# Kernel optimization log

Measured on AMD Instinct MI355X. Metric: run time of the kernel, lower is better.

## Reference

```python
import jax, jax.numpy as jnp
import numpy as np

B, N, H, W = 128, 8192, 7, 7


def setup_inputs() -> dict:
    key = jax.random.key(0)
    ks = jax.random.split(key, 10)
    inp = {
        'x': jax.random.normal(ks[0], (B, N, H, W), dtype=jnp.float32),
        'y': jax.random.normal(ks[1], (B, N), dtype=jnp.float32),
        # nn.MultiheadAttention(embed_dim=1, num_heads=1) params (all scalar)
        'wq': jax.random.normal(ks[2], (), dtype=jnp.float32),
        'wk': jax.random.normal(ks[3], (), dtype=jnp.float32),
        'wv': jax.random.normal(ks[4], (), dtype=jnp.float32),
        'bq': jax.random.normal(ks[5], (), dtype=jnp.float32) * 0.1,
        'bk': jax.random.normal(ks[6], (), dtype=jnp.float32) * 0.1,
        'bv': jax.random.normal(ks[7], (), dtype=jnp.float32) * 0.1,
        'wo': jax.random.normal(ks[8], (), dtype=jnp.float32),
        'bo': jax.random.normal(ks[9], (), dtype=jnp.float32) * 0.1,
    }
    return inp


def _mha1(q_src, kv_src, wq, bq, wk, bk, wv, bv, wo, bo):
    # embed_dim=1, num_heads=1, scale = 1/sqrt(1) = 1.
    # torch sees (seq=B, batch=N, embed=1): attention mixes the B axis per n.
    q = q_src * wq + bq            # [B, N]
    k = kv_src * wk + bk           # [B, N]
    v = kv_src * wv + bv           # [B, N]
    scores = jnp.einsum('in,jn->ijn', q, k)      # [B, B, N]
    a = jax.nn.softmax(scores, axis=1)           # softmax over keys j
    out = jnp.einsum('ijn,jn->in', a, v)         # [B, N]
    return out * wo + bo


def reference(x, y, wq, bq, wk, bk, wv, bv, wo, bo):
    xp = jnp.mean(x, axis=(2, 3))                # AdaptiveAvgPool2d((1,1)) -> [B, N]
    self_x = _mha1(xp, xp, wq, bq, wk, bk, wv, bv, wo, bo)
    self_y = _mha1(y, y, wq, bq, wk, bk, wv, bv, wo, bo)
    cross_x = _mha1(xp, y, wq, bq, wk, bk, wv, bv, wo, bo)
    cross_y = _mha1(y, xp, wq, bq, wk, bk, wv, bv, wo, bo)
    f_x = xp + self_x
    f_y = y + self_y
    c_f_x = cross_x + f_x
    c_f_y = cross_y + f_y
    return jnp.concatenate((c_f_x, c_f_y), axis=1)   # [B, 2N]
```

## Files before the change

kernel.cpp:

```cpp
#include <hip/hip_runtime.h>


constexpr int B_SEQ = 128;
constexpr int N_COL = 8192;
constexpr int HWP   = 49;
constexpr int NT    = 256;
constexpr int TC    = 4;
constexpr int VSTR  = 132;
constexpr int OSTR  = 5;

typedef float v2f __attribute__((ext_vector_type(2)));

#if __has_builtin(__builtin_elementwise_fma)
#define VFMA(a, b, c) __builtin_elementwise_fma((a), (b), (c))
#else
__device__ __forceinline__ v2f VFMA(v2f a, v2f b, v2f c) {
    v2f r; r.x = fmaf(a.x, b.x, c.x); r.y = fmaf(a.y, b.y, c.y); return r;
}
#endif

__global__ __launch_bounds__(NT, 5) void rsca_fused(
    const float* __restrict__ x, const float* __restrict__ y,
    const float* __restrict__ pwq, const float* __restrict__ pwk,
    const float* __restrict__ pwv, const float* __restrict__ pbq,
    const float* __restrict__ pbk, const float* __restrict__ pbv,
    const float* __restrict__ pwo, const float* __restrict__ pbo,
    float* __restrict__ out)
{
    __shared__ float xv[TC * VSTR];
    __shared__ float yv[TC * VSTR];
    __shared__ float pmnx[8][TC], pmxx[8][TC];
    __shared__ float pmny[4][TC], pmxy[4][TC];
    __shared__ float obuf[2][B_SEQ * OSTR];

    const int t    = threadIdx.x;
    const int bid  = blockIdx.x;
    const int cg = (bid & 7) * ((N_COL / TC) >> 3) + (bid >> 3);
    const int n0 = cg * TC;

    const int ql   = t & 3;
    const int seg  = t >> 2;
    const int lane = t & 63;
    const int wid  = t >> 6;

    const float wq = pwq[0], wk = pwk[0], wv = pwv[0];
    const float bq = pbq[0], bk = pbk[0], bv = pbv[0];
    const float wo = pwo[0], bo = pbo[0];
    const float L2E = 1.4426950408889634f;
    const float wkL = wk * L2E, bkL = bk * L2E;
    const float alpha = wo * wv;
    const float beta2 = 2.0f * (wo * bv + bo);

    {
        const int j = t >> 2, c = t & 3;
        const float fy0 = y[(size_t)j * N_COL + n0 + c];
        const float fy1 = y[(size_t)(j + 64) * N_COL + n0 + c];
        yv[c * VSTR + j]      = fy0;
        yv[c * VSTR + j + 64] = fy1;
        float mn = fminf(fy0, fy1), mx = fmaxf(fy0, fy1);
        #pragma unroll
        for (int off = 4; off <= 32; off <<= 1) {
            mn = fminf(mn, __shfl_xor(mn, off));
            mx = fmaxf(mx, __shfl_xor(mx, off));
        }
        if (lane < 4) { pmny[wid][lane] = mn; pmxy[wid][lane] = mx; }
    }

    for (int pass = 0; pass < 2; ++pass) {
        const int j = pass * 64 + seg;
        const float4* __restrict__ base =
            (const float4*)(x + ((size_t)j * N_COL + n0) * (size_t)HWP);
        float4 v[13];
        #pragma unroll
        for (int k = 0; k < 12; ++k) v[k] = base[ql + 4 * k];
        v[12] = base[48];

        float s0 = 0.f, s1 = 0.f, s2 = 0.f, s3 = 0.f;
        s0 += v[0].x + v[0].y + v[0].z + v[0].w;
        s0 += v[1].x + v[1].y + v[1].z + v[1].w;
        s0 += v[2].x + v[2].y + v[2].z + v[2].w;
        s1 += v[4].x + v[4].y + v[4].z + v[4].w;
        s1 += v[5].x + v[5].y + v[5].z + v[5].w;
        s2 += v[7].x + v[7].y + v[7].z + v[7].w;
        s2 += v[8].x + v[8].y + v[8].z + v[8].w;
        s3 += v[10].x + v[10].y + v[10].z + v[10].w;
        s3 += v[11].x + v[11].y + v[11].z + v[11].w;
        { const float sm = v[3].x + v[3].y + v[3].z + v[3].w;
          const float cr = (ql == 0) ? v[3].x : 0.0f;
          s0 += cr; s1 += sm - cr; }
        { const float sm = v[6].x + v[6].y + v[6].z + v[6].w;
          const float cr = (ql == 0) ? (v[6].x + v[6].y) : 0.0f;
          s1 += cr; s2 += sm - cr; }
        { const float sm = v[9].x + v[9].y + v[9].z + v[9].w;
          const float cr = (ql == 0) ? (v[9].x + v[9].y + v[9].z) : 0.0f;
          s2 += cr; s3 += sm - cr; }
        const float tail = v[12].x + v[12].y + v[12].z + v[12].w;

        s0 += __shfl_xor(s0, 1); s1 += __shfl_xor(s1, 1);
        s2 += __shfl_xor(s2, 1); s3 += __shfl_xor(s3, 1);
        s0 += __shfl_xor(s0, 2); s1 += __shfl_xor(s1, 2);
        s2 += __shfl_xor(s2, 2); s3 += __shfl_xor(s3, 2);
        float r = s0;
        r = (ql == 1) ? s1 : r;
        r = (ql == 2) ? s2 : r;
        r = (ql == 3) ? (s3 + tail) : r;
        const float mean = r * (1.0f / HWP);
        xv[ql * VSTR + j] = mean;

        float mn = mean, mx = mean;
        #pragma unroll
        for (int off = 4; off <= 32; off <<= 1) {
            mn = fminf(mn, __shfl_xor(mn, off));
            mx = fmaxf(mx, __shfl_xor(mx, off));
        }
        if (lane < 4) {
            pmnx[pass * 4 + wid][lane] = mn;
            pmxx[pass * 4 + wid][lane] = mx;
        }
    }
    __syncthreads();

    const int i  = t & (B_SEQ - 1);
    const int ch = t >> 7;
    #pragma unroll
    for (int cc = 0; cc < 2; ++cc) {
        const int c = ch * 2 + cc;
        const float* __restrict__ vx = &xv[c * VSTR];
        const float* __restrict__ vy = &yv[c * VSTR];

        float vxmn = pmnx[0][c], vxmx = pmxx[0][c];
        #pragma unroll
        for (int s = 1; s < 8; ++s) {
            vxmn = fminf(vxmn, pmnx[s][c]);
            vxmx = fmaxf(vxmx, pmxx[s][c]);
        }
        float vymn = pmny[0][c], vymx = pmxy[0][c];
        #pragma unroll
        for (int s = 1; s < 4; ++s) {
            vymn = fminf(vymn, pmny[s][c]);
            vymx = fmaxf(vymx, pmxy[s][c]);
        }
        const float axv = fmaf(vxmx, wkL, bkL), bxv = fmaf(vxmn, wkL, bkL);
        const float kxmx = fmaxf(axv, bxv), kxmn = fminf(axv, bxv);
        const float ayv = fmaf(vymx, wkL, bkL), byv = fmaf(vymn, wkL, bkL);
        const float kymx = fmaxf(ayv, byv), kymn = fminf(ayv, byv);

        const float xi = vx[i], yi = vy[i];
        const float qx = fmaf(xi, wq, bq), qy = fmaf(yi, wq, bq);
        const float nmsx = -(qx >= 0.f ? qx * kxmx : qx * kxmn);
        const float nmcy = -(qy >= 0.f ? qy * kxmx : qy * kxmn);
        const float nmsy = -(qy >= 0.f ? qy * kymx : qy * kymn);
        const float nmcx = -(qx >= 0.f ? qx * kymx : qx * kymn);

        const float qxw = qx * wkL, qyw = qy * wkL;
        const v2f qxw2 = {qxw, qxw}, qyw2 = {qyw, qyw};
        const float csx = fmaf(qx, bkL, nmsx), ccy = fmaf(qy, bkL, nmcy);
        const float csy = fmaf(qy, bkL, nmsy), ccx = fmaf(qx, bkL, nmcx);
        const v2f csx2 = {csx, csx}, ccy2 = {ccy, ccy};
        const v2f csy2 = {csy, csy}, ccx2 = {ccx, ccx};

        v2f s0sx = {0.f, 0.f}, s1sx = {0.f, 0.f};
        v2f s0cy = {0.f, 0.f}, s1cy = {0.f, 0.f};
        v2f s0sy = {0.f, 0.f}, s1sy = {0.f, 0.f};
        v2f s0cx = {0.f, 0.f}, s1cx = {0.f, 0.f};

        auto px2 = [&](float v0, float v1) {
            const v2f vvj = {v0, v1};
            v2f t1 = VFMA(qxw2, vvj, csx2);
            v2f e1; e1.x = __builtin_amdgcn_exp2f(t1.x);
                    e1.y = __builtin_amdgcn_exp2f(t1.y);
            s1sx = VFMA(e1, vvj, s1sx); s0sx += e1;
            v2f t2 = VFMA(qyw2, vvj, ccy2);
            v2f e2; e2.x = __builtin_amdgcn_exp2f(t2.x);
                    e2.y = __builtin_amdgcn_exp2f(t2.y);
            s1cy = VFMA(e2, vvj, s1cy); s0cy += e2;
        };
        auto py2 = [&](float v0, float v1) {
            const v2f vvj = {v0, v1};
            v2f t3 = VFMA(qyw2, vvj, csy2);
            v2f e3; e3.x = __builtin_amdgcn_exp2f(t3.x);
                    e3.y = __builtin_amdgcn_exp2f(t3.y);
            s1sy = VFMA(e3, vvj, s1sy); s0sy += e3;
            v2f t4 = VFMA(qxw2, vvj, ccx2);
            v2f e4; e4.x = __builtin_amdgcn_exp2f(t4.x);
                    e4.y = __builtin_amdgcn_exp2f(t4.y);
            s1cx = VFMA(e4, vvj, s1cx); s0cx += e4;
        };

        float4 a0 = *(const float4*)&vx[0], a1 = *(const float4*)&vx[4];
        float4 b0 = *(const float4*)&vy[0], b1 = *(const float4*)&vy[4];
        for (int j0 = 0; j0 < B_SEQ; j0 += 8) {
            const int jn = (j0 + 8) & (B_SEQ - 1);
            float4 na0 = *(const float4*)&vx[jn];
            float4 na1 = *(const float4*)&vx[jn + 4];
            float4 nb0 = *(const float4*)&vy[jn];
            float4 nb1 = *(const float4*)&vy[jn + 4];

            px2(a0.x, a0.y); px2(a0.z, a0.w); px2(a1.x, a1.y); px2(a1.z, a1.w);
            py2(b0.x, b0.y); py2(b0.z, b0.w); py2(b1.x, b1.y); py2(b1.z, b1.w);

            a0 = na0; a1 = na1; b0 = nb0; b1 = nb1;
        }
        const float S0sx = s0sx.x + s0sx.y, S1sx = s1sx.x + s1sx.y;
        const float S0cy = s0cy.x + s0cy.y, S1cy = s1cy.x + s1cy.y;
        const float S0sy = s0sy.x + s0sy.y, S1sy = s1sy.x + s1sy.y;
        const float S0cx = s0cx.x + s0cx.y, S1cx = s1cx.x + s1cx.y;
        const float mx_attn = S1sx * __builtin_amdgcn_rcpf(S0sx)
                            + S1cx * __builtin_amdgcn_rcpf(S0cx);
        const float my_attn = S1sy * __builtin_amdgcn_rcpf(S0sy)
                            + S1cy * __builtin_amdgcn_rcpf(S0cy);
        obuf[0][i * OSTR + c] = fmaf(alpha, mx_attn, beta2 + xi);
        obuf[1][i * OSTR + c] = fmaf(alpha, my_attn, beta2 + yi);
    }
    __syncthreads();

    {
        const int set = t >> 7;
        const int ii  = t & (B_SEQ - 1);
        const float* p = &obuf[set][ii * OSTR];
        float4 val;
        val.x = p[0]; val.y = p[1]; val.z = p[2]; val.w = p[3];
        *(float4*)&out[(size_t)ii * (2 * N_COL) + (size_t)set * N_COL + n0] = val;
    }
}

extern "C" void kernel_launch(void* const* d_in, const int* in_sizes, int n_in,
                              void* d_out, int out_size, void* d_ws, size_t ws_size,
                              hipStream_t stream) {
    const float* x   = (const float*)d_in[0];
    const float* y   = (const float*)d_in[1];
    const float* pwq = (const float*)d_in[2];
    const float* pwk = (const float*)d_in[3];
    const float* pwv = (const float*)d_in[4];
    const float* pbq = (const float*)d_in[5];
    const float* pbk = (const float*)d_in[6];
    const float* pbv = (const float*)d_in[7];
    const float* pwo = (const float*)d_in[8];
    const float* pbo = (const float*)d_in[9];
    float* out = (float*)d_out;

    rsca_fused<<<dim3(N_COL / TC), dim3(NT), 0, stream>>>(
        x, y, pwq, pwk, pwv, pbq, pbk, pbv, pwo, pbo, out);
}
```

Measured before the change: 322.9 us.

## Warp-specialize kernel into producer load waves and consumer attention waves

Each 512-thread block now handles two 4-column groups. Four producer wavefronts load and pool x and y into double-buffered shared memory and signal readiness through workgroup-scope atomic counters. Four consumer wavefronts spin-wait on those counters, compute the attention sums, and write the outputs. The aim is to overlap global-memory loads with the exp-heavy softmax compute inside one block. In exchange it uses spin-wait synchronization, fewer blocks, and lower per-block occupancy, and because each buffer is used only once the overlap is limited to the two groups.

```diff
diff --git a/kernel.cpp b/kernel.cpp
--- a/kernel.cpp
+++ b/kernel.cpp
@@ -4,8 +4,10 @@
 constexpr int B_SEQ = 128;
 constexpr int N_COL = 8192;
 constexpr int HWP   = 49;
-constexpr int NT    = 256;
+constexpr int NT    = 512;
 constexpr int TC    = 4;
+constexpr int NG    = 2;
+constexpr int CPB   = TC * NG;
 constexpr int VSTR  = 132;
 constexpr int OSTR  = 5;
 
@@ -19,7 +21,7 @@
 }
 #endif
 
-__global__ __launch_bounds__(NT, 5) void rsca_fused(
+__global__ __launch_bounds__(NT, 4) void rsca_ws(
     const float* __restrict__ x, const float* __restrict__ y,
     const float* __restrict__ pwq, const float* __restrict__ pwk,
     const float* __restrict__ pwv, const float* __restrict__ pbq,
@@ -27,21 +29,21 @@
     const float* __restrict__ pwo, const float* __restrict__ pbo,
     float* __restrict__ out)
 {
-    __shared__ float xv[TC * VSTR];
-    __shared__ float yv[TC * VSTR];
-    __shared__ float pmnx[8][TC], pmxx[8][TC];
-    __shared__ float pmny[4][TC], pmxy[4][TC];
-    __shared__ float obuf[2][B_SEQ * OSTR];
+    __shared__ float kvx[2][TC * VSTR];
+    __shared__ float kvy[2][TC * VSTR];
+    __shared__ float pmnx[2][8][TC], pmxx[2][8][TC];
+    __shared__ float pmny[2][4][TC], pmxy[2][4][TC];
+    __shared__ float obuf[2][2][B_SEQ * OSTR];
+    __shared__ int   rdy[2], dne[2];
 
     const int t    = threadIdx.x;
     const int bid  = blockIdx.x;
-    const int cg = (bid & 7) * ((N_COL / TC) >> 3) + (bid >> 3);
-    const int n0 = cg * TC;
-
-    const int ql   = t & 3;
-    const int seg  = t >> 2;
     const int lane = t & 63;
-    const int wid  = t >> 6;
+    const int cg = (bid & 7) * ((N_COL / CPB) >> 3) + (bid >> 3);
+    const int n0 = cg * CPB;
+
+    if (t == 0) { rdy[0] = rdy[1] = 0; dne[0] = dne[1] = 0; }
+    __syncthreads();
 
     const float wq = pwq[0], wk = pwk[0], wv = pwv[0];
     const float bq = pbq[0], bk = pbk[0], bv = pbv[0];
@@ -51,176 +53,203 @@
     const float alpha = wo * wv;
     const float beta2 = 2.0f * (wo * bv + bo);
 
-    {
-        const int j = t >> 2, c = t & 3;
-        const float fy0 = y[(size_t)j * N_COL + n0 + c];
-        const float fy1 = y[(size_t)(j + 64) * N_COL + n0 + c];
-        yv[c * VSTR + j]      = fy0;
-        yv[c * VSTR + j + 64] = fy1;
-        float mn = fminf(fy0, fy1), mx = fmaxf(fy0, fy1);
+    if (t < 256) {
+        const int ql  = t & 3;
+        const int seg = t >> 2;
+        const int wid = t >> 6;
+        for (int g = 0; g < NG; ++g) {
+            const int s  = g & 1;
+            const int c0 = n0 + g * TC;
+            {
+                const float fy0 = y[(size_t)seg * N_COL + c0 + ql];
+                const float fy1 = y[(size_t)(seg + 64) * N_COL + c0 + ql];
+                kvy[s][ql * VSTR + seg]      = fy0;
+                kvy[s][ql * VSTR + seg + 64] = fy1;
+                float mn = fminf(fy0, fy1), mx = fmaxf(fy0, fy1);
+                #pragma unroll
+                for (int off = 4; off <= 32; off <<= 1) {
+                    mn = fminf(mn, __shfl_xor(mn, off));
+                    mx = fmaxf(mx, __shfl_xor(mx, off));
+                }
+                if (lane < 4) { pmny[s][wid][lane] = mn; pmxy[s][wid][lane] = mx; }
+            }
+            for (int pass = 0; pass < 2; ++pass) {
+                const int j = pass * 64 + seg;
+                const float4* __restrict__ base =
+                    (const float4*)(x + ((size_t)j * N_COL + c0) * (size_t)HWP);
+                float4 v[13];
+                #pragma unroll
+                for (int k = 0; k < 12; ++k) v[k] = base[ql + 4 * k];
+                v[12] = base[48];
+
+                float s0 = 0.f, s1 = 0.f, s2 = 0.f, s3 = 0.f;
+                s0 += v[0].x + v[0].y + v[0].z + v[0].w;
+                s0 += v[1].x + v[1].y + v[1].z + v[1].w;
+                s0 += v[2].x + v[2].y + v[2].z + v[2].w;
+                s1 += v[4].x + v[4].y + v[4].z + v[4].w;
+                s1 += v[5].x + v[5].y + v[5].z + v[5].w;
+                s2 += v[7].x + v[7].y + v[7].z + v[7].w;
+                s2 += v[8].x + v[8].y + v[8].z + v[8].w;
+                s3 += v[10].x + v[10].y + v[10].z + v[10].w;
+                s3 += v[11].x + v[11].y + v[11].z + v[11].w;
+                { const float sm = v[3].x + v[3].y + v[3].z + v[3].w;
+                  const float cr = (ql == 0) ? v[3].x : 0.0f;
+                  s0 += cr; s1 += sm - cr; }
+                { const float sm = v[6].x + v[6].y + v[6].z + v[6].w;
+                  const float cr = (ql == 0) ? (v[6].x + v[6].y) : 0.0f;
+                  s1 += cr; s2 += sm - cr; }
+                { const float sm = v[9].x + v[9].y + v[9].z + v[9].w;
+                  const float cr = (ql == 0) ? (v[9].x + v[9].y + v[9].z) : 0.0f;
+                  s2 += cr; s3 += sm - cr; }
+                const float tail = v[12].x + v[12].y + v[12].z + v[12].w;
+
+                s0 += __shfl_xor(s0, 1); s1 += __shfl_xor(s1, 1);
+                s2 += __shfl_xor(s2, 1); s3 += __shfl_xor(s3, 1);
+                s0 += __shfl_xor(s0, 2); s1 += __shfl_xor(s1, 2);
+                s2 += __shfl_xor(s2, 2); s3 += __shfl_xor(s3, 2);
+                float r = s0;
+                r = (ql == 1) ? s1 : r;
+                r = (ql == 2) ? s2 : r;
+                r = (ql == 3) ? (s3 + tail) : r;
+                const float mean = r * (1.0f / HWP);
+                kvx[s][ql * VSTR + j] = mean;
+
+                float mn = mean, mx = mean;
+                #pragma unroll
+                for (int off = 4; off <= 32; off <<= 1) {
+                    mn = fminf(mn, __shfl_xor(mn, off));
+                    mx = fmaxf(mx, __shfl_xor(mx, off));
+                }
+                if (lane < 4) {
+                    pmnx[s][pass * 4 + wid][lane] = mn;
+                    pmxx[s][pass * 4 + wid][lane] = mx;
+                }
+            }
+            if (lane == 0)
+                __hip_atomic_fetch_add(&rdy[s], 1, __ATOMIC_RELEASE,
+                                       __HIP_MEMORY_SCOPE_WORKGROUP);
+        }
+    } else {
+        const int tc = t - 256;
+        const int i  = tc & (B_SEQ - 1);
+        const int ch = tc >> 7;
+        for (int g = 0; g < NG; ++g) {
+            const int s   = g & 1;
+            const int tgt = 4 * (g / 2 + 1);
+            while (__hip_atomic_load(&rdy[s], __ATOMIC_ACQUIRE,
+                                     __HIP_MEMORY_SCOPE_WORKGROUP) < tgt)
+                __builtin_amdgcn_s_sleep(2);
+
+            #pragma unroll
+            for (int cc = 0; cc < 2; ++cc) {
+                const int c = ch * 2 + cc;
+                const float* __restrict__ vx = &kvx[s][c * VSTR];
+                const float* __restrict__ vy = &kvy[s][c * VSTR];
+
+                float vxmn = pmnx[s][0][c], vxmx = pmxx[s][0][c];
+                #pragma unroll
+                for (int p = 1; p < 8; ++p) {
+                    vxmn = fminf(vxmn, pmnx[s][p][c]);
+                    vxmx = fmaxf(vxmx, pmxx[s][p][c]);
+                }
+                float vymn = pmny[s][0][c], vymx = pmxy[s][0][c];
+                #pragma unroll
+                for (int p = 1; p < 4; ++p) {
+                    vymn = fminf(vymn, pmny[s][p][c]);
+                    vymx = fmaxf(vymx, pmxy[s][p][c]);
+                }
+                const float axv = fmaf(vxmx, wkL, bkL), bxv = fmaf(vxmn, wkL, bkL);
+                const float kxmx = fmaxf(axv, bxv), kxmn = fminf(axv, bxv);
+                const float ayv = fmaf(vymx, wkL, bkL), byv = fmaf(vymn, wkL, bkL);
+                const float kymx = fmaxf(ayv, byv), kymn = fminf(ayv, byv);
+
+                const float xi = vx[i], yi = vy[i];
+                const float qx = fmaf(xi, wq, bq), qy = fmaf(yi, wq, bq);
+                const float nmsx = -(qx >= 0.f ? qx * kxmx : qx * kxmn);
+                const float nmcy = -(qy >= 0.f ? qy * kxmx : qy * kxmn);
+                const float nmsy = -(qy >= 0.f ? qy * kymx : qy * kymn);
+                const float nmcx = -(qx >= 0.f ? qx * kymx : qx * kymn);
+
+                const float qxw = qx * wkL, qyw = qy * wkL;
+                const v2f qxw2 = {qxw, qxw}, qyw2 = {qyw, qyw};
+                const float csx = fmaf(qx, bkL, nmsx), ccy = fmaf(qy, bkL, nmcy);
+                const float csy = fmaf(qy, bkL, nmsy), ccx = fmaf(qx, bkL, nmcx);
+                const v2f csx2 = {csx, csx}, ccy2 = {ccy, ccy};
+                const v2f csy2 = {csy, csy}, ccx2 = {ccx, ccx};
+
+                v2f s0sx = {0.f, 0.f}, s1sx = {0.f, 0.f};
+                v2f s0cy = {0.f, 0.f}, s1cy = {0.f, 0.f};
+                v2f s0sy = {0.f, 0.f}, s1sy = {0.f, 0.f};
+                v2f s0cx = {0.f, 0.f}, s1cx = {0.f, 0.f};
+
+                auto px2 = [&](float v0, float v1) {
+                    const v2f vvj = {v0, v1};
+                    v2f t1 = VFMA(qxw2, vvj, csx2);
+                    v2f e1; e1.x = __builtin_amdgcn_exp2f(t1.x);
+                            e1.y = __builtin_amdgcn_exp2f(t1.y);
+                    s1sx = VFMA(e1, vvj, s1sx); s0sx += e1;
+                    v2f t2 = VFMA(qyw2, vvj, ccy2);
+                    v2f e2; e2.x = __builtin_amdgcn_exp2f(t2.x);
+                            e2.y = __builtin_amdgcn_exp2f(t2.y);
+                    s1cy = VFMA(e2, vvj, s1cy); s0cy += e2;
+                };
+                auto py2 = [&](float v0, float v1) {
+                    const v2f vvj = {v0, v1};
+                    v2f t3 = VFMA(qyw2, vvj, csy2);
+                    v2f e3; e3.x = __builtin_amdgcn_exp2f(t3.x);
+                            e3.y = __builtin_amdgcn_exp2f(t3.y);
+                    s1sy = VFMA(e3, vvj, s1sy); s0sy += e3;
+                    v2f t4 = VFMA(qxw2, vvj, ccx2);
+                    v2f e4; e4.x = __builtin_amdgcn_exp2f(t4.x);
+                            e4.y = __builtin_amdgcn_exp2f(t4.y);
+                    s1cx = VFMA(e4, vvj, s1cx); s0cx += e4;
+                };
+
+                float4 a0 = *(const float4*)&vx[0], a1 = *(const float4*)&vx[4];
+                float4 b0 = *(const float4*)&vy[0], b1 = *(const float4*)&vy[4];
+                for (int j0 = 0; j0 < B_SEQ; j0 += 8) {
+                    const int jn = (j0 + 8) & (B_SEQ - 1);
+                    float4 na0 = *(const float4*)&vx[jn];
+                    float4 na1 = *(const float4*)&vx[jn + 4];
+                    float4 nb0 = *(const float4*)&vy[jn];
+                    float4 nb1 = *(const float4*)&vy[jn + 4];
+
+                    px2(a0.x, a0.y); px2(a0.z, a0.w); px2(a1.x, a1.y); px2(a1.z, a1.w);
+                    py2(b0.x, b0.y); py2(b0.z, b0.w); py2(b1.x, b1.y); py2(b1.z, b1.w);
+
+                    a0 = na0; a1 = na1; b0 = nb0; b1 = nb1;
+                }
+                const float S0sx = s0sx.x + s0sx.y, S1sx = s1sx.x + s1sx.y;
+                const float S0cy = s0cy.x + s0cy.y, S1cy = s1cy.x + s1cy.y;
+                const float S0sy = s0sy.x + s0sy.y, S1sy = s1sy.x + s1sy.y;
+                const float S0cx = s0cx.x + s0cx.y, S1cx = s1cx.x + s1cx.y;
+                const float mx_attn = S1sx * __builtin_amdgcn_rcpf(S0sx)
+                                    + S1cx * __builtin_amdgcn_rcpf(S0cx);
+                const float my_attn = S1sy * __builtin_amdgcn_rcpf(S0sy)
+                                    + S1cy * __builtin_amdgcn_rcpf(S0cy);
+                obuf[s][0][i * OSTR + c] = fmaf(alpha, mx_attn, beta2 + xi);
+                obuf[s][1][i * OSTR + c] = fmaf(alpha, my_attn, beta2 + yi);
+            }
+            if (lane == 0)
+                __hip_atomic_fetch_add(&dne[s], 1, __ATOMIC_RELEASE,
+                                       __HIP_MEMORY_SCOPE_WORKGROUP);
+        }
+        while (__hip_atomic_load(&dne[0], __ATOMIC_ACQUIRE,
+                                 __HIP_MEMORY_SCOPE_WORKGROUP) < 4)
+            __builtin_amdgcn_s_sleep(1);
+        while (__hip_atomic_load(&dne[1], __ATOMIC_ACQUIRE,
+                                 __HIP_MEMORY_SCOPE_WORKGROUP) < 4)
+            __builtin_amdgcn_s_sleep(1);
+        const int set = tc >> 7;
+        const int ii  = tc & (B_SEQ - 1);
         #pragma unroll
-        for (int off = 4; off <= 32; off <<= 1) {
-            mn = fminf(mn, __shfl_xor(mn, off));
-            mx = fmaxf(mx, __shfl_xor(mx, off));
+        for (int s = 0; s < NG; ++s) {
+            const float* p = &obuf[s][set][ii * OSTR];
+            float4 val;
+            val.x = p[0]; val.y = p[1]; val.z = p[2]; val.w = p[3];
+            *(float4*)&out[(size_t)ii * (2 * N_COL) + (size_t)set * N_COL
+                           + n0 + s * TC] = val;
         }
-        if (lane < 4) { pmny[wid][lane] = mn; pmxy[wid][lane] = mx; }
-    }
-
-    for (int pass = 0; pass < 2; ++pass) {
-        const int j = pass * 64 + seg;
-        const float4* __restrict__ base =
-            (const float4*)(x + ((size_t)j * N_COL + n0) * (size_t)HWP);
-        float4 v[13];
-        #pragma unroll
-        for (int k = 0; k < 12; ++k) v[k] = base[ql + 4 * k];
-        v[12] = base[48];
-
-        float s0 = 0.f, s1 = 0.f, s2 = 0.f, s3 = 0.f;
-        s0 += v[0].x + v[0].y + v[0].z + v[0].w;
-        s0 += v[1].x + v[1].y + v[1].z + v[1].w;
-        s0 += v[2].x + v[2].y + v[2].z + v[2].w;
-        s1 += v[4].x + v[4].y + v[4].z + v[4].w;
-        s1 += v[5].x + v[5].y + v[5].z + v[5].w;
-        s2 += v[7].x + v[7].y + v[7].z + v[7].w;
-        s2 += v[8].x + v[8].y + v[8].z + v[8].w;
-        s3 += v[10].x + v[10].y + v[10].z + v[10].w;
-        s3 += v[11].x + v[11].y + v[11].z + v[11].w;
-        { const float sm = v[3].x + v[3].y + v[3].z + v[3].w;
-          const float cr = (ql == 0) ? v[3].x : 0.0f;
-          s0 += cr; s1 += sm - cr; }
-        { const float sm = v[6].x + v[6].y + v[6].z + v[6].w;
-          const float cr = (ql == 0) ? (v[6].x + v[6].y) : 0.0f;
-          s1 += cr; s2 += sm - cr; }
-        { const float sm = v[9].x + v[9].y + v[9].z + v[9].w;
-          const float cr = (ql == 0) ? (v[9].x + v[9].y + v[9].z) : 0.0f;
-          s2 += cr; s3 += sm - cr; }
-        const float tail = v[12].x + v[12].y + v[12].z + v[12].w;
-
-        s0 += __shfl_xor(s0, 1); s1 += __shfl_xor(s1, 1);
-        s2 += __shfl_xor(s2, 1); s3 += __shfl_xor(s3, 1);
-        s0 += __shfl_xor(s0, 2); s1 += __shfl_xor(s1, 2);
-        s2 += __shfl_xor(s2, 2); s3 += __shfl_xor(s3, 2);
-        float r = s0;
-        r = (ql == 1) ? s1 : r;
-        r = (ql == 2) ? s2 : r;
-        r = (ql == 3) ? (s3 + tail) : r;
-        const float mean = r * (1.0f / HWP);
-        xv[ql * VSTR + j] = mean;
-
-        float mn = mean, mx = mean;
-        #pragma unroll
-        for (int off = 4; off <= 32; off <<= 1) {
-            mn = fminf(mn, __shfl_xor(mn, off));
-            mx = fmaxf(mx, __shfl_xor(mx, off));
-        }
-        if (lane < 4) {
-            pmnx[pass * 4 + wid][lane] = mn;
-            pmxx[pass * 4 + wid][lane] = mx;
-        }
-    }
-    __syncthreads();
-
-    const int i  = t & (B_SEQ - 1);
-    const int ch = t >> 7;
-    #pragma unroll
-    for (int cc = 0; cc < 2; ++cc) {
-        const int c = ch * 2 + cc;
-        const float* __restrict__ vx = &xv[c * VSTR];
-        const float* __restrict__ vy = &yv[c * VSTR];
-
-        float vxmn = pmnx[0][c], vxmx = pmxx[0][c];
-        #pragma unroll
-        for (int s = 1; s < 8; ++s) {
-            vxmn = fminf(vxmn, pmnx[s][c]);
-            vxmx = fmaxf(vxmx, pmxx[s][c]);
-        }
-        float vymn = pmny[0][c], vymx = pmxy[0][c];
-        #pragma unroll
-        for (int s = 1; s < 4; ++s) {
-            vymn = fminf(vymn, pmny[s][c]);
-            vymx = fmaxf(vymx, pmxy[s][c]);
-        }
-        const float axv = fmaf(vxmx, wkL, bkL), bxv = fmaf(vxmn, wkL, bkL);
-        const float kxmx = fmaxf(axv, bxv), kxmn = fminf(axv, bxv);
-        const float ayv = fmaf(vymx, wkL, bkL), byv = fmaf(vymn, wkL, bkL);
-        const float kymx = fmaxf(ayv, byv), kymn = fminf(ayv, byv);
-
-        const float xi = vx[i], yi = vy[i];
-        const float qx = fmaf(xi, wq, bq), qy = fmaf(yi, wq, bq);
-        const float nmsx = -(qx >= 0.f ? qx * kxmx : qx * kxmn);
-        const float nmcy = -(qy >= 0.f ? qy * kxmx : qy * kxmn);
-        const float nmsy = -(qy >= 0.f ? qy * kymx : qy * kymn);
-        const float nmcx = -(qx >= 0.f ? qx * kymx : qx * kymn);
-
-        const float qxw = qx * wkL, qyw = qy * wkL;
-        const v2f qxw2 = {qxw, qxw}, qyw2 = {qyw, qyw};
-        const float csx = fmaf(qx, bkL, nmsx), ccy = fmaf(qy, bkL, nmcy);
-        const float csy = fmaf(qy, bkL, nmsy), ccx = fmaf(qx, bkL, nmcx);
-        const v2f csx2 = {csx, csx}, ccy2 = {ccy, ccy};
-        const v2f csy2 = {csy, csy}, ccx2 = {ccx, ccx};
-
-        v2f s0sx = {0.f, 0.f}, s1sx = {0.f, 0.f};
-        v2f s0cy = {0.f, 0.f}, s1cy = {0.f, 0.f};
-        v2f s0sy = {0.f, 0.f}, s1sy = {0.f, 0.f};
-        v2f s0cx = {0.f, 0.f}, s1cx = {0.f, 0.f};
-
-        auto px2 = [&](float v0, float v1) {
-            const v2f vvj = {v0, v1};
-            v2f t1 = VFMA(qxw2, vvj, csx2);
-            v2f e1; e1.x = __builtin_amdgcn_exp2f(t1.x);
-                    e1.y = __builtin_amdgcn_exp2f(t1.y);
-            s1sx = VFMA(e1, vvj, s1sx); s0sx += e1;
-            v2f t2 = VFMA(qyw2, vvj, ccy2);
-            v2f e2; e2.x = __builtin_amdgcn_exp2f(t2.x);
-                    e2.y = __builtin_amdgcn_exp2f(t2.y);
-            s1cy = VFMA(e2, vvj, s1cy); s0cy += e2;
-        };
-        auto py2 = [&](float v0, float v1) {
-            const v2f vvj = {v0, v1};
-            v2f t3 = VFMA(qyw2, vvj, csy2);
-            v2f e3; e3.x = __builtin_amdgcn_exp2f(t3.x);
-                    e3.y = __builtin_amdgcn_exp2f(t3.y);
-            s1sy = VFMA(e3, vvj, s1sy); s0sy += e3;
-            v2f t4 = VFMA(qxw2, vvj, ccx2);
-            v2f e4; e4.x = __builtin_amdgcn_exp2f(t4.x);
-                    e4.y = __builtin_amdgcn_exp2f(t4.y);
-            s1cx = VFMA(e4, vvj, s1cx); s0cx += e4;
-        };
-
-        float4 a0 = *(const float4*)&vx[0], a1 = *(const float4*)&vx[4];
-        float4 b0 = *(const float4*)&vy[0], b1 = *(const float4*)&vy[4];
-        for (int j0 = 0; j0 < B_SEQ; j0 += 8) {
-            const int jn = (j0 + 8) & (B_SEQ - 1);
-            float4 na0 = *(const float4*)&vx[jn];
-            float4 na1 = *(const float4*)&vx[jn + 4];
-            float4 nb0 = *(const float4*)&vy[jn];
-            float4 nb1 = *(const float4*)&vy[jn + 4];
-
-            px2(a0.x, a0.y); px2(a0.z, a0.w); px2(a1.x, a1.y); px2(a1.z, a1.w);
-            py2(b0.x, b0.y); py2(b0.z, b0.w); py2(b1.x, b1.y); py2(b1.z, b1.w);
-
-            a0 = na0; a1 = na1; b0 = nb0; b1 = nb1;
-        }
-        const float S0sx = s0sx.x + s0sx.y, S1sx = s1sx.x + s1sx.y;
-        const float S0cy = s0cy.x + s0cy.y, S1cy = s1cy.x + s1cy.y;
-        const float S0sy = s0sy.x + s0sy.y, S1sy = s1sy.x + s1sy.y;
-        const float S0cx = s0cx.x + s0cx.y, S1cx = s1cx.x + s1cx.y;
-        const float mx_attn = S1sx * __builtin_amdgcn_rcpf(S0sx)
-                            + S1cx * __builtin_amdgcn_rcpf(S0cx);
-        const float my_attn = S1sy * __builtin_amdgcn_rcpf(S0sy)
-                            + S1cy * __builtin_amdgcn_rcpf(S0cy);
-        obuf[0][i * OSTR + c] = fmaf(alpha, mx_attn, beta2 + xi);
-        obuf[1][i * OSTR + c] = fmaf(alpha, my_attn, beta2 + yi);
-    }
-    __syncthreads();
-
-    {
-        const int set = t >> 7;
-        const int ii  = t & (B_SEQ - 1);
-        const float* p = &obuf[set][ii * OSTR];
-        float4 val;
-        val.x = p[0]; val.y = p[1]; val.z = p[2]; val.w = p[3];
-        *(float4*)&out[(size_t)ii * (2 * N_COL) + (size_t)set * N_COL + n0] = val;
     }
 }
 
@@ -239,6 +268,6 @@
     const float* pbo = (const float*)d_in[9];
     float* out = (float*)d_out;
 
-    rsca_fused<<<dim3(N_COL / TC), dim3(NT), 0, stream>>>(
+    rsca_ws<<<dim3(N_COL / CPB), dim3(NT), 0, stream>>>(
         x, y, pwq, pwk, pwv, pbq, pbk, pbv, pwo, pbo, out);
 }
```

New measurement: 324.4 us. Within noise of the previous version (+0.5%).

## Stagger x pooling and y self-attention across blocks by parity

Applied to the files above, without the earlier changes.

Moves the self-y attention, which depends only on y, into its own loop. Blocks with odd parity (by bid>>8) run it before pooling x, while even-parity blocks pool x first. The aim is that blocks resident together do not all load x from HBM at once and then all compute exponentials at once, so memory and ALU phases overlap. In exchange the y-attention values must be carried in registers until the end, and the y loop runs twice as two narrower loops.

```diff
diff --git a/kernel.cpp b/kernel.cpp
--- a/kernel.cpp
+++ b/kernel.cpp
@@ -37,6 +37,7 @@
     const int bid  = blockIdx.x;
     const int cg = (bid & 7) * ((N_COL / TC) >> 3) + (bid >> 3);
     const int n0 = cg * TC;
+    const int par = (bid >> 8) & 1;
 
     const int ql   = t & 3;
     const int seg  = t >> 2;
@@ -66,62 +67,118 @@
         if (lane < 4) { pmny[wid][lane] = mn; pmxy[wid][lane] = mx; }
     }
 
-    for (int pass = 0; pass < 2; ++pass) {
-        const int j = pass * 64 + seg;
-        const float4* __restrict__ base =
-            (const float4*)(x + ((size_t)j * N_COL + n0) * (size_t)HWP);
-        float4 v[13];
-        #pragma unroll
-        for (int k = 0; k < 12; ++k) v[k] = base[ql + 4 * k];
-        v[12] = base[48];
-
-        float s0 = 0.f, s1 = 0.f, s2 = 0.f, s3 = 0.f;
-        s0 += v[0].x + v[0].y + v[0].z + v[0].w;
-        s0 += v[1].x + v[1].y + v[1].z + v[1].w;
-        s0 += v[2].x + v[2].y + v[2].z + v[2].w;
-        s1 += v[4].x + v[4].y + v[4].z + v[4].w;
-        s1 += v[5].x + v[5].y + v[5].z + v[5].w;
-        s2 += v[7].x + v[7].y + v[7].z + v[7].w;
-        s2 += v[8].x + v[8].y + v[8].z + v[8].w;
-        s3 += v[10].x + v[10].y + v[10].z + v[10].w;
-        s3 += v[11].x + v[11].y + v[11].z + v[11].w;
-        { const float sm = v[3].x + v[3].y + v[3].z + v[3].w;
-          const float cr = (ql == 0) ? v[3].x : 0.0f;
-          s0 += cr; s1 += sm - cr; }
-        { const float sm = v[6].x + v[6].y + v[6].z + v[6].w;
-          const float cr = (ql == 0) ? (v[6].x + v[6].y) : 0.0f;
-          s1 += cr; s2 += sm - cr; }
-        { const float sm = v[9].x + v[9].y + v[9].z + v[9].w;
-          const float cr = (ql == 0) ? (v[9].x + v[9].y + v[9].z) : 0.0f;
-          s2 += cr; s3 += sm - cr; }
-        const float tail = v[12].x + v[12].y + v[12].z + v[12].w;
-
-        s0 += __shfl_xor(s0, 1); s1 += __shfl_xor(s1, 1);
-        s2 += __shfl_xor(s2, 1); s3 += __shfl_xor(s3, 1);
-        s0 += __shfl_xor(s0, 2); s1 += __shfl_xor(s1, 2);
-        s2 += __shfl_xor(s2, 2); s3 += __shfl_xor(s3, 2);
-        float r = s0;
-        r = (ql == 1) ? s1 : r;
-        r = (ql == 2) ? s2 : r;
-        r = (ql == 3) ? (s3 + tail) : r;
-        const float mean = r * (1.0f / HWP);
-        xv[ql * VSTR + j] = mean;
-
-        float mn = mean, mx = mean;
-        #pragma unroll
-        for (int off = 4; off <= 32; off <<= 1) {
-            mn = fminf(mn, __shfl_xor(mn, off));
-            mx = fmaxf(mx, __shfl_xor(mx, off));
-        }
-        if (lane < 4) {
-            pmnx[pass * 4 + wid][lane] = mn;
-            pmxx[pass * 4 + wid][lane] = mx;
-        }
-    }
-    __syncthreads();
+    auto pool_x = [&]() {
+        for (int pass = 0; pass < 2; ++pass) {
+            const int j = pass * 64 + seg;
+            const float4* __restrict__ base =
+                (const float4*)(x + ((size_t)j * N_COL + n0) * (size_t)HWP);
+            float4 v[13];
+            #pragma unroll
+            for (int k = 0; k < 12; ++k) v[k] = base[ql + 4 * k];
+            v[12] = base[48];
+
+            float s0 = 0.f, s1 = 0.f, s2 = 0.f, s3 = 0.f;
+            s0 += v[0].x + v[0].y + v[0].z + v[0].w;
+            s0 += v[1].x + v[1].y + v[1].z + v[1].w;
+            s0 += v[2].x + v[2].y + v[2].z + v[2].w;
+            s1 += v[4].x + v[4].y + v[4].z + v[4].w;
+            s1 += v[5].x + v[5].y + v[5].z + v[5].w;
+            s2 += v[7].x + v[7].y + v[7].z + v[7].w;
+            s2 += v[8].x + v[8].y + v[8].z + v[8].w;
+            s3 += v[10].x + v[10].y + v[10].z + v[10].w;
+            s3 += v[11].x + v[11].y + v[11].z + v[11].w;
+            { const float sm = v[3].x + v[3].y + v[3].z + v[3].w;
+              const float cr = (ql == 0) ? v[3].x : 0.0f;
+              s0 += cr; s1 += sm - cr; }
+            { const float sm = v[6].x + v[6].y + v[6].z + v[6].w;
+              const float cr = (ql == 0) ? (v[6].x + v[6].y) : 0.0f;
+              s1 += cr; s2 += sm - cr; }
+            { const float sm = v[9].x + v[9].y + v[9].z + v[9].w;
+              const float cr = (ql == 0) ? (v[9].x + v[9].y + v[9].z) : 0.0f;
+              s2 += cr; s3 += sm - cr; }
+            const float tail = v[12].x + v[12].y + v[12].z + v[12].w;
+
+            s0 += __shfl_xor(s0, 1); s1 += __shfl_xor(s1, 1);
+            s2 += __shfl_xor(s2, 1); s3 += __shfl_xor(s3, 1);
+            s0 += __shfl_xor(s0, 2); s1 += __shfl_xor(s1, 2);
+            s2 += __shfl_xor(s2, 2); s3 += __shfl_xor(s3, 2);
+            float r = s0;
+            r = (ql == 1) ? s1 : r;
+            r = (ql == 2) ? s2 : r;
+            r = (ql == 3) ? (s3 + tail) : r;
+            const float mean = r * (1.0f / HWP);
+            xv[ql * VSTR + j] = mean;
+
+            float mn = mean, mx = mean;
+            #pragma unroll
+            for (int off = 4; off <= 32; off <<= 1) {
+                mn = fminf(mn, __shfl_xor(mn, off));
+                mx = fmaxf(mx, __shfl_xor(mx, off));
+            }
+            if (lane < 4) {
+                pmnx[pass * 4 + wid][lane] = mn;
+                pmxx[pass * 4 + wid][lane] = mx;
+            }
+        }
+    };
 
     const int i  = t & (B_SEQ - 1);
     const int ch = t >> 7;
+
+    if (par == 0) {
+        pool_x();
+        __syncthreads();
+    } else {
+        __syncthreads();
+    }
+
+    v2f syS0[2], syS1[2];
+    #pragma unroll
+    for (int cc = 0; cc < 2; ++cc) {
+        const int c = ch * 2 + cc;
+        const float* __restrict__ vy = &yv[c * VSTR];
+        float vymn = pmny[0][c], vymx = pmxy[0][c];
+        #pragma unroll
+        for (int s = 1; s < 4; ++s) {
+            vymn = fminf(vymn, pmny[s][c]);
+            vymx = fmaxf(vymx, pmxy[s][c]);
+        }
+        const float ayv = fmaf(vymx, wkL, bkL), byv = fmaf(vymn, wkL, bkL);
+        const float kymx = fmaxf(ayv, byv), kymn = fminf(ayv, byv);
+
+        const float yi = vy[i];
+        const float qy = fmaf(yi, wq, bq);
+        const float nmsy = -(qy >= 0.f ? qy * kymx : qy * kymn);
+        const float qyw = qy * wkL;
+        const v2f qyw2 = {qyw, qyw};
+        const float csy = fmaf(qy, bkL, nmsy);
+        const v2f csy2 = {csy, csy};
+
+        v2f s0 = {0.f, 0.f}, s1 = {0.f, 0.f};
+        auto pairY = [&](float v0, float v1) {
+            const v2f vvj = {v0, v1};
+            v2f t3 = VFMA(qyw2, vvj, csy2);
+            v2f e3; e3.x = __builtin_amdgcn_exp2f(t3.x);
+                    e3.y = __builtin_amdgcn_exp2f(t3.y);
+            s1 = VFMA(e3, vvj, s1); s0 += e3;
+        };
+        float4 b0 = *(const float4*)&vy[0], b1 = *(const float4*)&vy[4];
+        for (int j0 = 0; j0 < B_SEQ; j0 += 8) {
+            const int jn = (j0 + 8) & (B_SEQ - 1);
+            float4 nb0 = *(const float4*)&vy[jn];
+            float4 nb1 = *(const float4*)&vy[jn + 4];
+            pairY(b0.x, b0.y); pairY(b0.z, b0.w);
+            pairY(b1.x, b1.y); pairY(b1.z, b1.w);
+            b0 = nb0; b1 = nb1;
+        }
+        syS0[cc] = s0; syS1[cc] = s1;
+    }
+
+    if (par == 1) {
+        pool_x();
+        __syncthreads();
+    }
+
     #pragma unroll
     for (int cc = 0; cc < 2; ++cc) {
         const int c = ch * 2 + cc;
@@ -149,22 +206,19 @@
         const float qx = fmaf(xi, wq, bq), qy = fmaf(yi, wq, bq);
         const float nmsx = -(qx >= 0.f ? qx * kxmx : qx * kxmn);
         const float nmcy = -(qy >= 0.f ? qy * kxmx : qy * kxmn);
-        const float nmsy = -(qy >= 0.f ? qy * kymx : qy * kymn);
         const float nmcx = -(qx >= 0.f ? qx * kymx : qx * kymn);
 
         const float qxw = qx * wkL, qyw = qy * wkL;
         const v2f qxw2 = {qxw, qxw}, qyw2 = {qyw, qyw};
         const float csx = fmaf(qx, bkL, nmsx), ccy = fmaf(qy, bkL, nmcy);
-        const float csy = fmaf(qy, bkL, nmsy), ccx = fmaf(qx, bkL, nmcx);
-        const v2f csx2 = {csx, csx}, ccy2 = {ccy, ccy};
-        const v2f csy2 = {csy, csy}, ccx2 = {ccx, ccx};
+        const float ccx = fmaf(qx, bkL, nmcx);
+        const v2f csx2 = {csx, csx}, ccy2 = {ccy, ccy}, ccx2 = {ccx, ccx};
 
         v2f s0sx = {0.f, 0.f}, s1sx = {0.f, 0.f};
         v2f s0cy = {0.f, 0.f}, s1cy = {0.f, 0.f};
-        v2f s0sy = {0.f, 0.f}, s1sy = {0.f, 0.f};
         v2f s0cx = {0.f, 0.f}, s1cx = {0.f, 0.f};
 
-        auto px2 = [&](float v0, float v1) {
+        auto pairX = [&](float v0, float v1) {
             const v2f vvj = {v0, v1};
             v2f t1 = VFMA(qxw2, vvj, csx2);
             v2f e1; e1.x = __builtin_amdgcn_exp2f(t1.x);
@@ -175,12 +229,8 @@
                     e2.y = __builtin_amdgcn_exp2f(t2.y);
             s1cy = VFMA(e2, vvj, s1cy); s0cy += e2;
         };
-        auto py2 = [&](float v0, float v1) {
+        auto pairW = [&](float v0, float v1) {
             const v2f vvj = {v0, v1};
-            v2f t3 = VFMA(qyw2, vvj, csy2);
-            v2f e3; e3.x = __builtin_amdgcn_exp2f(t3.x);
-                    e3.y = __builtin_amdgcn_exp2f(t3.y);
-            s1sy = VFMA(e3, vvj, s1sy); s0sy += e3;
             v2f t4 = VFMA(qxw2, vvj, ccx2);
             v2f e4; e4.x = __builtin_amdgcn_exp2f(t4.x);
                     e4.y = __builtin_amdgcn_exp2f(t4.y);
@@ -196,15 +246,18 @@
             float4 nb0 = *(const float4*)&vy[jn];
             float4 nb1 = *(const float4*)&vy[jn + 4];
 
-            px2(a0.x, a0.y); px2(a0.z, a0.w); px2(a1.x, a1.y); px2(a1.z, a1.w);
-            py2(b0.x, b0.y); py2(b0.z, b0.w); py2(b1.x, b1.y); py2(b1.z, b1.w);
+            pairX(a0.x, a0.y); pairX(a0.z, a0.w);
+            pairX(a1.x, a1.y); pairX(a1.z, a1.w);
+            pairW(b0.x, b0.y); pairW(b0.z, b0.w);
+            pairW(b1.x, b1.y); pairW(b1.z, b1.w);
 
             a0 = na0; a1 = na1; b0 = nb0; b1 = nb1;
         }
         const float S0sx = s0sx.x + s0sx.y, S1sx = s1sx.x + s1sx.y;
         const float S0cy = s0cy.x + s0cy.y, S1cy = s1cy.x + s1cy.y;
-        const float S0sy = s0sy.x + s0sy.y, S1sy = s1sy.x + s1sy.y;
         const float S0cx = s0cx.x + s0cx.y, S1cx = s1cx.x + s1cx.y;
+        const float S0sy = syS0[cc].x + syS0[cc].y;
+        const float S1sy = syS1[cc].x + syS1[cc].y;
         const float mx_attn = S1sx * __builtin_amdgcn_rcpf(S0sx)
                             + S1cx * __builtin_amdgcn_rcpf(S0cx);
         const float my_attn = S1sy * __builtin_amdgcn_rcpf(S0sy)
```

Measured after the change: 318.8 us. No clear change (-1.3%).
